# Kernel optimization log

Hardware: AMD Instinct MI355X
Metric: run time of the kernel (lower is better)

The kernel has to match this reference:

```python
import jax, jax.numpy as jnp
import numpy as np

B, S, DN, L = 2048, 8, 8, 50        # batch, n_sparse, n_dense, hist len
V, VF = 100000, 100000              # sparse vocab, feed vocab
ED, FD = 16, 512                    # sparse embed dim, feed embed dim
HID1, HID2 = 256, 128               # DNN hidden sizes
NE, NT, EO = 8, 4, 8                # experts, tasks, expert out dim
INPUT_DIM = ED * S + DN + FD + FD   # 1160


def setup_inputs() -> dict:
    key = jax.random.key(0)
    ks = jax.random.split(key, 20)
    sc = 0.02
    f32 = jnp.float32
    return {
        "sparse_ids": jax.random.randint(ks[0], (B, S), 0, V),
        "dense": jax.random.normal(ks[1], (B, DN), f32),
        "feedid": jax.random.randint(ks[2], (B,), 0, VF),
        "hist_feedid": jax.random.randint(ks[3], (B, L), 0, VF),
        "emb_tables": jax.random.normal(ks[4], (S, V, ED), f32) * sc,
        "feed_table": jax.random.normal(ks[5], (VF, FD), f32) * sc,
        "attn_w1": jax.random.normal(ks[6], (4 * FD, 128), f32) * sc,
        "attn_b1": jnp.zeros((128,), f32),
        "attn_w2": jax.random.normal(ks[7], (128, 1), f32) * sc,
        "attn_b2": jnp.zeros((1,), f32),
        "dnn_w1": jax.random.normal(ks[8], (INPUT_DIM, HID1), f32) * sc,
        "dnn_b1": jnp.zeros((HID1,), f32),
        "dnn_w2": jax.random.normal(ks[9], (HID1, HID2), f32) * sc,
        "dnn_b2": jnp.zeros((HID2,), f32),
        "expert_w": jax.random.normal(ks[10], (NE, HID2, EO), f32) * sc,
        "gate_w": jax.random.normal(ks[11], (NT, HID2, NE), f32) * sc,
        "out_w": jax.random.normal(ks[12], (NT, EO, 1), f32) * sc,
        "out_b": jnp.zeros((NT, 1), f32),
    }


def reference(sparse_ids, dense, feedid, hist_feedid,
              emb_tables, feed_table,
              attn_w1, attn_b1, attn_w2, attn_b2,
              dnn_w1, dnn_b1, dnn_w2, dnn_b2,
              expert_w, gate_w, out_w, out_b):
    # --- sparse embeddings: one table per feature -> [B, S, ED] -> flat ---
    embed = jax.vmap(lambda t, ids: t[ids], in_axes=(0, 1), out_axes=1)(
        emb_tables, sparse_ids)                       # [B, S, ED]
    sparse_flat = embed.reshape(embed.shape[0], -1)   # [B, S*ED]

    # --- feed / history embeddings ---
    feed = feed_table[feedid]                         # [B, FD]
    hist = feed_table[hist_feedid]                    # [B, L, FD]

    # --- DIN attention (query=feed, keys=hist) ---
    q = jnp.broadcast_to(feed[:, None, :], hist.shape)          # [B, L, FD]
    x = jnp.concatenate([q, hist, q - hist, q * hist], axis=-1)  # [B, L, 4FD]
    h = jax.nn.relu(x @ attn_w1 + attn_b1)                       # [B, L, 128]
    scores = (h @ attn_w2 + attn_b2)[..., 0]                     # [B, L]
    attn = jax.nn.softmax(scores, axis=1)
    user_interest = jnp.einsum('bl,bld->bd', attn, hist)         # [B, FD]

    # --- DNN (dropout off in eval) ---
    dnn_in = jnp.concatenate([sparse_flat, dense, feed, user_interest], axis=1)
    z = jax.nn.relu(dnn_in @ dnn_w1 + dnn_b1)
    dnn_out = jax.nn.relu(z @ dnn_w2 + dnn_b2)                   # [B, 128]

    # --- MMOE (eval: no expert dropout mask) ---
    expert_out = jnp.einsum('bi,eio->beo', dnn_out, expert_w)    # [B, NE, EO]
    gates = jax.nn.softmax(jnp.einsum('bi,tie->bte', dnn_out, gate_w), axis=-1)
    task_out = jnp.einsum('bte,beo->bto', gates, expert_out)     # [B, NT, EO]

    # --- per-task heads ---
    logits = jnp.einsum('bto,toh->bth', task_out, out_w) + out_b  # [B, NT, 1]
    return jax.nn.sigmoid(logits)
```

## Files before the change

### kernel.cpp

```cpp
#include <hip/hip_runtime.h>
#include <hip/hip_bf16.h>

typedef unsigned short u16;
typedef unsigned int u32;
typedef __attribute__((ext_vector_type(8))) short short8;
typedef __attribute__((ext_vector_type(8))) u16 ushort8;
typedef __attribute__((ext_vector_type(4))) float f32x4;

#define BB 2048
#define SS 8
#define DNUM 8
#define LL 50
#define EDIM 16
#define FDIM 512
#define HID1 256
#define HID2 128
#define VF 100000
#define KDNN 1216
#define ROWS (BB*LL)

__device__ inline u16 f2bf(float x) {
    return __builtin_bit_cast(u16, __float2bfloat16(x));
}
__device__ inline float bf2f(u16 b) {
    u32 u = ((u32)b) << 16;
    return __builtin_bit_cast(float, u);
}
__device__ inline void load16_lds(const void* g, void* l) {
    __builtin_amdgcn_global_load_lds(
        (const __attribute__((address_space(1))) u32*)g,
        (__attribute__((address_space(3))) u32*)l, 16, 0, 0);
}
__device__ inline float wave_sum(float v) {
    #pragma unroll
    for (int off = 32; off > 0; off >>= 1) v += __shfl_xor(v, off, 64);
    return v;
}
__device__ inline float wave_max(float v) {
    #pragma unroll
    for (int off = 32; off > 0; off >>= 1) v = fmaxf(v, __shfl_xor(v, off, 64));
    return v;
}
__device__ inline void cvt8(const float4& a, const float4& b, ushort8& o) {
    o[0]=f2bf(a.x); o[1]=f2bf(a.y); o[2]=f2bf(a.z); o[3]=f2bf(a.w);
    o[4]=f2bf(b.x); o[5]=f2bf(b.y); o[6]=f2bf(b.z); o[7]=f2bf(b.w);
}

__global__ __launch_bounds__(256) void zero_flags(u32* __restrict__ f) {
    int i = blockIdx.x * 256 + threadIdx.x;
    if (i < 25024) f[i] = 0;
}

__global__ __launch_bounds__(256) void mark_used(
    const int* __restrict__ hist, const int* __restrict__ feedid,
    unsigned char* __restrict__ flags)
{
    int i = blockIdx.x * 256 + threadIdx.x;
    if (i < ROWS) flags[hist[i]] = 1;
    if (i < BB) flags[feedid[i]] = 1;
}

#define CVT_BLKS 25000
#define PREP_BLKS 2112
__global__ __launch_bounds__(256) void prep_all(
    const float* __restrict__ ft, u16* __restrict__ hb,
    const unsigned char* __restrict__ flags,
    const float* __restrict__ w1, const float* __restrict__ dw1,
    const float* __restrict__ dw2,
    u16* __restrict__ WHP_T, u16* __restrict__ WQ_T,
    u16* __restrict__ W1D_T, u16* __restrict__ W2D_T,
    const int* __restrict__ sparse_ids, const float* __restrict__ dense,
    const int* __restrict__ feedid, const float* __restrict__ emb_tables,
    u16* __restrict__ dnn_in, u16* __restrict__ A_q)
{
    int blk = blockIdx.x, t = threadIdx.x;
    if (blk < CVT_BLKS) {
        int r = blk * 4 + (t >> 6);
        if (flags[r]) {
            const float* src = ft + (size_t)r * FDIM + (t & 63) * 8;
            float4 a = *(const float4*)src;
            float4 b = *(const float4*)(src + 4);
            ushort8 o; cvt8(a, b, o);
            *(ushort8*)(hb + (size_t)r * FDIM + (t & 63) * 8) = o;
        }
    } else if (blk < CVT_BLKS + PREP_BLKS) {
        int idx = (blk - CVT_BLKS) * 256 + t;
        if (idx < 131072) {
            int n = idx >> 10, k = idx & 1023;
            float v;
            if (k < 512) v = w1[(512 + k) * 128 + n] - w1[(1024 + k) * 128 + n];
            else         v = w1[(1024 + k) * 128 + n];
            WHP_T[n * 1024 + k] = f2bf(v);
        } else if (idx < 196608) {
            int i = idx - 131072;
            int n = i >> 9, k = i & 511;
            WQ_T[n * 512 + k] = f2bf(w1[k * 128 + n] + w1[(1024 + k) * 128 + n]);
        } else if (idx < 507904) {
            int i = idx - 196608;
            int n = i / KDNN, k = i - n * KDNN;
            W1D_T[i] = (k < 1160) ? f2bf(dw1[k * HID1 + n]) : (u16)0;
        } else if (idx < 540672) {
            int i = idx - 507904;
            int n = i >> 8, k = i & 255;
            W2D_T[i] = f2bf(dw2[k * HID2 + n]);
        }
    } else {
        int b = blk - (CVT_BLKS + PREP_BLKS);
        u16* drow = dnn_in + (size_t)b * KDNN;
        if (t < 128) {
            int s = t >> 4, e = t & 15;
            int id = sparse_ids[b * SS + s];
            float v = emb_tables[(size_t)s * 1600000 + (size_t)id * EDIM + e];
            drow[t] = f2bf(v);
        } else if (t < 136) {
            drow[t] = f2bf(dense[b * DNUM + (t - 128)]);
        } else if (t < 192) {
            drow[1160 + (t - 136)] = 0;
        }
        int fid = feedid[b];
        float2 f = *(const float2*)&ft[(size_t)fid * FDIM + t * 2];
        u16 u0 = f2bf(f.x), u1 = f2bf(f.y);
        drow[136 + t * 2] = u0;
        drow[136 + t * 2 + 1] = u1;
        A_q[(size_t)b * FDIM + t * 2] = u0;
        A_q[(size_t)b * FDIM + t * 2 + 1] = u1;
    }
}

template<int BM, bool RELU, bool OUT_BF16>
__global__ __launch_bounds__(256, 4) void gemm_bt(
    const u16* __restrict__ A, int lda,
    const u16* __restrict__ BT, int ldb,
    const float* __restrict__ bias,
    void* __restrict__ Cv, int M, int N, int K)
{
    constexpr int MI = BM / 32;
    __shared__ u16 As[BM * 64];
    __shared__ u16 Bs[128 * 64];
    int m0 = blockIdx.x * BM, n0 = blockIdx.y * 128;
    int tid = threadIdx.x, wave = tid >> 6, lane = tid & 63;
    int lrow = lane >> 3, lk = (lane & 7) * 8;
    f32x4 acc[MI][4];
    f32x4 zz = {0.f, 0.f, 0.f, 0.f};
    #pragma unroll
    for (int i = 0; i < MI; i++)
        #pragma unroll
        for (int j = 0; j < 4; j++) acc[i][j] = zz;
    int wm = (wave >> 1) * (BM / 2), wn = (wave & 1) * 64;

    for (int kt = 0; kt < K; kt += 64) {
        #pragma unroll
        for (int j = 0; j < MI; ++j) {
            int c = wave * MI + j;
            int row = c * 8 + lrow;
            load16_lds(A + (size_t)(m0 + row) * lda + kt + lk, &As[c * 512]);
        }
        #pragma unroll
        for (int j = 0; j < 4; ++j) {
            int c = wave * 4 + j;
            int row = c * 8 + lrow;
            load16_lds(BT + (size_t)(n0 + row) * ldb + kt + lk, &Bs[c * 512]);
        }
        __syncthreads();
        #pragma unroll
        for (int ks = 0; ks < 2; ++ks) {
            int kk = ks * 32 + (lane >> 4) * 8;
            short8 af[MI], bf[4];
            #pragma unroll
            for (int i = 0; i < MI; i++)
                af[i] = *(const short8*)&As[(wm + i * 16 + (lane & 15)) * 64 + kk];
            #pragma unroll
            for (int j = 0; j < 4; j++)
                bf[j] = *(const short8*)&Bs[(wn + j * 16 + (lane & 15)) * 64 + kk];
            #pragma unroll
            for (int i = 0; i < MI; i++)
                #pragma unroll
                for (int j = 0; j < 4; j++)
                    acc[i][j] = __builtin_amdgcn_mfma_f32_16x16x32_bf16(
                        af[i], bf[j], acc[i][j], 0, 0, 0);
        }
        __syncthreads();
    }
    #pragma unroll
    for (int i = 0; i < MI; i++) {
        #pragma unroll
        for (int j = 0; j < 4; j++) {
            #pragma unroll
            for (int r = 0; r < 4; r++) {
                int row = m0 + wm + i * 16 + (lane >> 4) * 4 + r;
                int col = n0 + wn + j * 16 + (lane & 15);
                float v = acc[i][j][r];
                if (bias) v += bias[col];
                if (RELU) v = fmaxf(v, 0.f);
                size_t off = (size_t)row * N + col;
                if (OUT_BF16) ((u16*)Cv)[off] = f2bf(v);
                else ((float*)Cv)[off] = v;
            }
        }
    }
}

#define MFMA_BF16 __builtin_amdgcn_mfma_f32_16x16x32_bf16

__global__ __launch_bounds__(256, 4) void din_gemm(
    const int* __restrict__ hist_ids, const int* __restrict__ feedid,
    const u16* __restrict__ HB, const u16* __restrict__ WHP_T,
    const float* __restrict__ qw, const float* __restrict__ b1,
    const float* __restrict__ w2v, float* __restrict__ scores)
{
    __shared__ u16 As[2][64 * 32];
    __shared__ u16 BsH[128 * 32];
    __shared__ u16 BsP[128 * 32];
    __shared__ u16 qls[3 * 512];
    __shared__ float qbs[3 * 128];
    __shared__ float w2s[128];
    __shared__ float sred[64 * 2];

    int t = threadIdx.x, w = t >> 6, lane = t & 63;
    int m0 = blockIdx.x * 64, b0 = m0 / LL;
    int fr = lane & 15, kg8 = (lane >> 4) * 8;
    int wm = (w >> 1) * 32, wn = (w & 1) * 64;

    for (int idx = t; idx < 384; idx += 256) {
        int bi = idx >> 7, col = idx & 127;
        int bb = b0 + bi; if (bb > BB - 1) bb = BB - 1;
        qbs[idx] = qw[bb * 128 + col] + b1[col];
    }
    if (t < 128) w2s[t] = w2v[t];

    const u16* a_src = HB + (size_t)hist_ids[m0 + w * 16 + (lane >> 2)] * FDIM
                          + (lane & 3) * 8;
    const u16* b_src0 = WHP_T + (size_t)(w * 32 + (lane >> 2)) * 1024 + (lane & 3) * 8;
    const u16* b_src1 = b_src0 + 16 * 1024;

    if (w < 3) {
        int bb = b0 + w; if (bb > BB - 1) bb = BB - 1;
        load16_lds(HB + (size_t)feedid[bb] * FDIM + lane * 8, &qls[w * 512]);
    }
    int qb0 = (m0 + wm + fr) / LL - b0;
    int qb1 = (m0 + wm + 16 + fr) / LL - b0;

    f32x4 acc[2][4];
    f32x4 zz = {0.f, 0.f, 0.f, 0.f};
    #pragma unroll
    for (int i = 0; i < 2; i++)
        #pragma unroll
        for (int j = 0; j < 4; j++) acc[i][j] = zz;

    load16_lds(a_src,         &As[0][w * 512]);
    load16_lds(b_src0,        &BsH[(w * 2) * 512]);
    load16_lds(b_src1,        &BsH[(w * 2 + 1) * 512]);
    load16_lds(b_src0 + 512,  &BsP[(w * 2) * 512]);
    load16_lds(b_src1 + 512,  &BsP[(w * 2 + 1) * 512]);
    load16_lds(a_src + 32,    &As[1][w * 512]);
    asm volatile("s_waitcnt vmcnt(1) lgkmcnt(0)" ::: "memory");
    __builtin_amdgcn_s_barrier();

    #pragma unroll
    for (int kt = 0; kt < 16; ++kt) {
        const int buf = kt & 1;
        const int ko = kt * 32;
        short8 ah0 = *(const short8*)&As[buf][(wm + fr) * 32 + kg8];
        short8 ah1 = *(const short8*)&As[buf][(wm + 16 + fr) * 32 + kg8];
        ushort8 qv0 = *(const ushort8*)&qls[qb0 * 512 + ko + kg8];
        ushort8 qv1 = *(const ushort8*)&qls[qb1 * 512 + ko + kg8];
        short8 bh[4], bp[4];
        #pragma unroll
        for (int j = 0; j < 4; ++j) {
            int n = wn + j * 16 + fr;
            bh[j] = *(const short8*)&BsH[n * 32 + kg8];
            bp[j] = *(const short8*)&BsP[n * 32 + kg8];
        }
        #pragma unroll
        for (int j = 0; j < 4; ++j) {
            acc[0][j] = MFMA_BF16(ah0, bh[j], acc[0][j], 0, 0, 0);
            acc[1][j] = MFMA_BF16(ah1, bh[j], acc[1][j], 0, 0, 0);
        }
        ushort8 hv0 = __builtin_bit_cast(ushort8, ah0);
        ushort8 hv1 = __builtin_bit_cast(ushort8, ah1);
        ushort8 pv0, pv1;
        #pragma unroll
        for (int e = 0; e < 8; ++e) {
            pv0[e] = f2bf(bf2f(hv0[e]) * bf2f(qv0[e]));
            pv1[e] = f2bf(bf2f(hv1[e]) * bf2f(qv1[e]));
        }
        short8 ap0 = __builtin_bit_cast(short8, pv0);
        short8 ap1 = __builtin_bit_cast(short8, pv1);
        #pragma unroll
        for (int j = 0; j < 4; ++j) {
            acc[0][j] = MFMA_BF16(ap0, bp[j], acc[0][j], 0, 0, 0);
            acc[1][j] = MFMA_BF16(ap1, bp[j], acc[1][j], 0, 0, 0);
        }
        asm volatile("s_waitcnt lgkmcnt(0)" ::: "memory");
        __builtin_amdgcn_s_barrier();
        if (kt < 15) {
            const int kn = (kt + 1) * 32;
            load16_lds(b_src0 + kn,       &BsH[(w * 2) * 512]);
            load16_lds(b_src1 + kn,       &BsH[(w * 2 + 1) * 512]);
            load16_lds(b_src0 + 512 + kn, &BsP[(w * 2) * 512]);
            load16_lds(b_src1 + 512 + kn, &BsP[(w * 2 + 1) * 512]);
            if (kt < 14) {
                load16_lds(a_src + (kt + 2) * 32, &As[buf][w * 512]);
                asm volatile("s_waitcnt vmcnt(1)" ::: "memory");
            } else {
                asm volatile("s_waitcnt vmcnt(0)" ::: "memory");
            }
            __builtin_amdgcn_s_barrier();
        }
    }

    #pragma unroll
    for (int i = 0; i < 2; ++i) {
        #pragma unroll
        for (int r = 0; r < 4; ++r) {
            int rl = wm + i * 16 + (lane >> 4) * 4 + r;
            int bi = (m0 + rl) / LL - b0;
            float s = 0.f;
            #pragma unroll
            for (int j = 0; j < 4; ++j) {
                int col = wn + j * 16 + fr;
                float v = acc[i][j][r] + qbs[bi * 128 + col];
                s += fmaxf(v, 0.f) * w2s[col];
            }
            s += __shfl_xor(s, 1, 64);
            s += __shfl_xor(s, 2, 64);
            s += __shfl_xor(s, 4, 64);
            s += __shfl_xor(s, 8, 64);
            if (fr == 0) sred[rl * 2 + (w & 1)] = s;
        }
    }
    __syncthreads();
    if (t < 64) scores[m0 + t] = sred[t * 2] + sred[t * 2 + 1];
}

__global__ __launch_bounds__(256) void softmax_ui(
    const float* __restrict__ scores, const int* __restrict__ hist_ids,
    const u16* __restrict__ HB, u16* __restrict__ dnn_in)
{
    int b = blockIdx.x, t = threadIdx.x;
    int wave = t >> 6, lane = t & 63;
    __shared__ float sc[56];
    __shared__ int hid[56];
    if (t >= 64 && t < 64 + LL) hid[t - 64] = hist_ids[b * LL + (t - 64)];
    if (wave == 0) {
        float x = (lane < LL) ? scores[b * LL + lane] : -1e30f;
        float mx = wave_max(x);
        float e = (lane < LL) ? __expf(x - mx) : 0.f;
        float s = wave_sum(e);
        if (lane < LL) sc[lane] = e / s;
    }
    __syncthreads();
    int d = t * 2;
    float a0 = 0.f, a1 = 0.f;
    #pragma unroll 5
    for (int l = 0; l < LL; ++l) {
        u32 v = *(const u32*)(HB + (size_t)hid[l] * FDIM + d);
        float al = sc[l];
        a0 += al * bf2f((u16)(v & 0xffff));
        a1 += al * bf2f((u16)(v >> 16));
    }
    dnn_in[(size_t)b * KDNN + 648 + d] = f2bf(a0);
    dnn_in[(size_t)b * KDNN + 648 + d + 1] = f2bf(a1);
}

__global__ __launch_bounds__(256) void mmoe_head(
    const float* __restrict__ dnn_out, const float* __restrict__ expert_w,
    const float* __restrict__ gate_w, const float* __restrict__ out_w,
    const float* __restrict__ out_b, float* __restrict__ out)
{
    int wave = threadIdx.x >> 6, lane = threadIdx.x & 63;
    int b = blockIdx.x * 4 + wave;
    __shared__ float ds[4][128];
    __shared__ float eo[4][64];
    __shared__ float gt[4][32];
    ds[wave][lane] = dnn_out[b * 128 + lane];
    ds[wave][lane + 64] = dnn_out[b * 128 + 64 + lane];
    __syncthreads();
    int e = lane >> 3, o = lane & 7;
    float acc = 0.f;
    for (int k = 0; k < 128; ++k)
        acc += ds[wave][k] * expert_w[(e * 128 + k) * 8 + o];
    eo[wave][lane] = acc;
    if (lane < 32) {
        int tt = lane >> 3, ee = lane & 7;
        float g = 0.f;
        for (int k = 0; k < 128; ++k)
            g += ds[wave][k] * gate_w[(tt * 128 + k) * 8 + ee];
        float m = g;
        #pragma unroll
        for (int off = 4; off; off >>= 1) m = fmaxf(m, __shfl_xor(m, off, 8));
        float ex = __expf(g - m);
        float s = ex;
        #pragma unroll
        for (int off = 4; off; off >>= 1) s += __shfl_xor(s, off, 8);
        gt[wave][lane] = ex / s;
    }
    __syncthreads();
    if (lane < 32) {
        int tt = lane >> 3, o2 = lane & 7;
        float to = 0.f;
        #pragma unroll
        for (int ee = 0; ee < 8; ++ee)
            to += gt[wave][tt * 8 + ee] * eo[wave][ee * 8 + o2];
        float pl = to * out_w[tt * 8 + o2];
        #pragma unroll
        for (int off = 4; off; off >>= 1) pl += __shfl_xor(pl, off, 8);
        if (o2 == 0) {
            float logit = pl + out_b[tt];
            out[b * 4 + tt] = 1.f / (1.f + __expf(-logit));
        }
    }
}

extern "C" void kernel_launch(void* const* d_in, const int* in_sizes, int n_in,
                              void* d_out, int out_size, void* d_ws, size_t ws_size,
                              hipStream_t stream)
{
    const int*   sparse_ids = (const int*)d_in[0];
    const float* dense      = (const float*)d_in[1];
    const int*   feedid     = (const int*)d_in[2];
    const int*   hist_ids   = (const int*)d_in[3];
    const float* emb_tables = (const float*)d_in[4];
    const float* feed_table = (const float*)d_in[5];
    const float* attn_w1    = (const float*)d_in[6];
    const float* attn_b1    = (const float*)d_in[7];
    const float* attn_w2    = (const float*)d_in[8];
    const float* attn_b2    = (const float*)d_in[9];
    const float* dnn_w1     = (const float*)d_in[10];
    const float* dnn_b1     = (const float*)d_in[11];
    const float* dnn_w2     = (const float*)d_in[12];
    const float* dnn_b2     = (const float*)d_in[13];
    const float* expert_w   = (const float*)d_in[14];
    const float* gate_w     = (const float*)d_in[15];
    const float* out_w      = (const float*)d_in[16];
    const float* out_b      = (const float*)d_in[17];
    float* out = (float*)d_out;

    char* ws = (char*)d_ws;
    size_t off = 0;
    auto alloc = [&](size_t bytes) {
        char* p = ws + off;
        off += (bytes + 255) & ~(size_t)255;
        return p;
    };
    u16* WHP_T = (u16*)alloc(131072 * 2);
    u16* WQ_T  = (u16*)alloc(65536 * 2);
    u16* W1D_T = (u16*)alloc((size_t)HID1 * KDNN * 2);
    u16* W2D_T = (u16*)alloc((size_t)HID2 * HID1 * 2);
    u16* AQ    = (u16*)alloc((size_t)BB * FDIM * 2);
    float* QW  = (float*)alloc((size_t)BB * 128 * 4);
    u16* DNNIN = (u16*)alloc((size_t)BB * KDNN * 2);
    u16* Z     = (u16*)alloc((size_t)BB * HID1 * 2);
    float* DOUT= (float*)alloc((size_t)BB * HID2 * 4);
    float* SCORES = (float*)alloc((size_t)ROWS * 4);
    unsigned char* FLAGS = (unsigned char*)alloc(100096);
    u16* HB16  = (u16*)alloc((size_t)VF * FDIM * 2);

    zero_flags<<<98, 256, 0, stream>>>((u32*)FLAGS);
    mark_used<<<400, 256, 0, stream>>>(hist_ids, feedid, FLAGS);
    prep_all<<<CVT_BLKS + PREP_BLKS + BB, 256, 0, stream>>>(
        feed_table, HB16, FLAGS, attn_w1, dnn_w1, dnn_w2,
        WHP_T, WQ_T, W1D_T, W2D_T,
        sparse_ids, dense, feedid, emb_tables, DNNIN, AQ);
    gemm_bt<32, false, false><<<dim3(BB / 32, 1), 256, 0, stream>>>(
        AQ, 512, WQ_T, 512, nullptr, QW, BB, 128, 512);
    din_gemm<<<ROWS / 64, 256, 0, stream>>>(
        hist_ids, feedid, HB16, WHP_T, QW, attn_b1, attn_w2, SCORES);
    softmax_ui<<<BB, 256, 0, stream>>>(SCORES, hist_ids, HB16, DNNIN);
    gemm_bt<32, true, true><<<dim3(BB / 32, HID1 / 128), 256, 0, stream>>>(
        DNNIN, KDNN, W1D_T, KDNN, dnn_b1, Z, BB, HID1, KDNN);
    gemm_bt<32, true, false><<<dim3(BB / 32, 1), 256, 0, stream>>>(
        Z, HID1, W2D_T, HID1, dnn_b2, DOUT, BB, HID2, HID1);
    mmoe_head<<<BB / 4, 256, 0, stream>>>(DOUT, expert_w, gate_w, out_w,
                                          out_b, out);
}
```

Baseline: 152.6 us.

## Gather fp32 feed rows directly in DIN GEMM instead of pre-converting table to bf16

Drops the flag-marking kernels and the pass that converted every used feed-table row to bf16 in a workspace copy. The DIN attention GEMM now streams fp32 history rows straight into LDS and converts them to bf16 in registers before the MFMA. The query rows and the softmax-weighted sum read the fp32 table too. This removes two launches and a large scan-and-write of the table, at the cost of twice the gather bytes per history row in the main GEMM and extra conversion work in its inner loop.

Result: no change. 150.2 us (-1.6%).

```diff
diff --git a/kernel.cpp b/kernel.cpp
--- a/kernel.cpp
+++ b/kernel.cpp
@@ -46,25 +46,9 @@
     o[4]=f2bf(b.x); o[5]=f2bf(b.y); o[6]=f2bf(b.z); o[7]=f2bf(b.w);
 }
 
-__global__ __launch_bounds__(256) void zero_flags(u32* __restrict__ f) {
-    int i = blockIdx.x * 256 + threadIdx.x;
-    if (i < 25024) f[i] = 0;
-}
-
-__global__ __launch_bounds__(256) void mark_used(
-    const int* __restrict__ hist, const int* __restrict__ feedid,
-    unsigned char* __restrict__ flags)
-{
-    int i = blockIdx.x * 256 + threadIdx.x;
-    if (i < ROWS) flags[hist[i]] = 1;
-    if (i < BB) flags[feedid[i]] = 1;
-}
-
-#define CVT_BLKS 25000
 #define PREP_BLKS 2112
-__global__ __launch_bounds__(256) void prep_all(
-    const float* __restrict__ ft, u16* __restrict__ hb,
-    const unsigned char* __restrict__ flags,
+__global__ __launch_bounds__(256) void prep_small(
+    const float* __restrict__ ft,
     const float* __restrict__ w1, const float* __restrict__ dw1,
     const float* __restrict__ dw2,
     u16* __restrict__ WHP_T, u16* __restrict__ WQ_T,
@@ -74,17 +58,8 @@
     u16* __restrict__ dnn_in, u16* __restrict__ A_q)
 {
     int blk = blockIdx.x, t = threadIdx.x;
-    if (blk < CVT_BLKS) {
-        int r = blk * 4 + (t >> 6);
-        if (flags[r]) {
-            const float* src = ft + (size_t)r * FDIM + (t & 63) * 8;
-            float4 a = *(const float4*)src;
-            float4 b = *(const float4*)(src + 4);
-            ushort8 o; cvt8(a, b, o);
-            *(ushort8*)(hb + (size_t)r * FDIM + (t & 63) * 8) = o;
-        }
-    } else if (blk < CVT_BLKS + PREP_BLKS) {
-        int idx = (blk - CVT_BLKS) * 256 + t;
+    if (blk < PREP_BLKS) {
+        int idx = blk * 256 + t;
         if (idx < 131072) {
             int n = idx >> 10, k = idx & 1023;
             float v;
@@ -105,7 +80,7 @@
             W2D_T[i] = f2bf(dw2[k * HID2 + n]);
         }
     } else {
-        int b = blk - (CVT_BLKS + PREP_BLKS);
+        int b = blk - PREP_BLKS;
         u16* drow = dnn_in + (size_t)b * KDNN;
         if (t < 128) {
             int s = t >> 4, e = t & 15;
@@ -204,11 +179,11 @@
 
 __global__ __launch_bounds__(256, 4) void din_gemm(
     const int* __restrict__ hist_ids, const int* __restrict__ feedid,
-    const u16* __restrict__ HB, const u16* __restrict__ WHP_T,
+    const float* __restrict__ ft, const u16* __restrict__ WHP_T,
     const float* __restrict__ qw, const float* __restrict__ b1,
     const float* __restrict__ w2v, float* __restrict__ scores)
 {
-    __shared__ u16 As[2][64 * 32];
+    __shared__ float Asf[2][64 * 32];
     __shared__ u16 BsH[128 * 32];
     __shared__ u16 BsP[128 * 32];
     __shared__ u16 qls[3 * 512];
@@ -227,16 +202,20 @@
         qbs[idx] = qw[bb * 128 + col] + b1[col];
     }
     if (t < 128) w2s[t] = w2v[t];
-
-    const u16* a_src = HB + (size_t)hist_ids[m0 + w * 16 + (lane >> 2)] * FDIM
-                          + (lane & 3) * 8;
+    for (int idx = t; idx < 768; idx += 256) {
+        int bi = idx >> 8, d2 = (idx & 255) * 2;
+        int bb = b0 + bi; if (bb > BB - 1) bb = BB - 1;
+        float2 qv = *(const float2*)&ft[(size_t)feedid[bb] * FDIM + d2];
+        qls[bi * 512 + d2] = f2bf(qv.x);
+        qls[bi * 512 + d2 + 1] = f2bf(qv.y);
+    }
+
+    const float* a_src0 = ft + (size_t)hist_ids[m0 + w * 16 + fr] * FDIM
+                             + (lane >> 4) * 4;
+    const float* a_src1 = a_src0 + 16;
     const u16* b_src0 = WHP_T + (size_t)(w * 32 + (lane >> 2)) * 1024 + (lane & 3) * 8;
     const u16* b_src1 = b_src0 + 16 * 1024;
 
-    if (w < 3) {
-        int bb = b0 + w; if (bb > BB - 1) bb = BB - 1;
-        load16_lds(HB + (size_t)feedid[bb] * FDIM + lane * 8, &qls[w * 512]);
-    }
     int qb0 = (m0 + wm + fr) / LL - b0;
     int qb1 = (m0 + wm + 16 + fr) / LL - b0;
 
@@ -247,21 +226,33 @@
         #pragma unroll
         for (int j = 0; j < 4; j++) acc[i][j] = zz;
 
-    load16_lds(a_src,         &As[0][w * 512]);
+    load16_lds(a_src0,        &Asf[0][w * 512]);
+    load16_lds(a_src1,        &Asf[0][w * 512 + 256]);
     load16_lds(b_src0,        &BsH[(w * 2) * 512]);
     load16_lds(b_src1,        &BsH[(w * 2 + 1) * 512]);
     load16_lds(b_src0 + 512,  &BsP[(w * 2) * 512]);
     load16_lds(b_src1 + 512,  &BsP[(w * 2 + 1) * 512]);
-    load16_lds(a_src + 32,    &As[1][w * 512]);
-    asm volatile("s_waitcnt vmcnt(1) lgkmcnt(0)" ::: "memory");
+    load16_lds(a_src0 + 32,   &Asf[1][w * 512]);
+    load16_lds(a_src1 + 32,   &Asf[1][w * 512 + 256]);
+    asm volatile("s_waitcnt vmcnt(2) lgkmcnt(0)" ::: "memory");
     __builtin_amdgcn_s_barrier();
+
+    int ws0 = wm >> 4;
+    int k4a = (lane >> 4) * 2;
+    int offA0 = ws0 * 512 + k4a * 64 + fr * 4;
+    int offA1 = (ws0 + 1) * 512 + k4a * 64 + fr * 4;
 
     #pragma unroll
     for (int kt = 0; kt < 16; ++kt) {
         const int buf = kt & 1;
         const int ko = kt * 32;
-        short8 ah0 = *(const short8*)&As[buf][(wm + fr) * 32 + kg8];
-        short8 ah1 = *(const short8*)&As[buf][(wm + 16 + fr) * 32 + kg8];
+        float4 h0a = *(const float4*)&Asf[buf][offA0];
+        float4 h0b = *(const float4*)&Asf[buf][offA0 + 64];
+        float4 h1a = *(const float4*)&Asf[buf][offA1];
+        float4 h1b = *(const float4*)&Asf[buf][offA1 + 64];
+        ushort8 hv0, hv1;
+        cvt8(h0a, h0b, hv0);
+        cvt8(h1a, h1b, hv1);
         ushort8 qv0 = *(const ushort8*)&qls[qb0 * 512 + ko + kg8];
         ushort8 qv1 = *(const ushort8*)&qls[qb1 * 512 + ko + kg8];
         short8 bh[4], bp[4];
@@ -271,13 +262,13 @@
             bh[j] = *(const short8*)&BsH[n * 32 + kg8];
             bp[j] = *(const short8*)&BsP[n * 32 + kg8];
         }
+        short8 ah0 = __builtin_bit_cast(short8, hv0);
+        short8 ah1 = __builtin_bit_cast(short8, hv1);
         #pragma unroll
         for (int j = 0; j < 4; ++j) {
             acc[0][j] = MFMA_BF16(ah0, bh[j], acc[0][j], 0, 0, 0);
             acc[1][j] = MFMA_BF16(ah1, bh[j], acc[1][j], 0, 0, 0);
         }
-        ushort8 hv0 = __builtin_bit_cast(ushort8, ah0);
-        ushort8 hv1 = __builtin_bit_cast(ushort8, ah1);
         ushort8 pv0, pv1;
         #pragma unroll
         for (int e = 0; e < 8; ++e) {
@@ -294,14 +285,16 @@
         asm volatile("s_waitcnt lgkmcnt(0)" ::: "memory");
         __builtin_amdgcn_s_barrier();
         if (kt < 15) {
-            const int kn = (kt + 1) * 32;
-            load16_lds(b_src0 + kn,       &BsH[(w * 2) * 512]);
-            load16_lds(b_src1 + kn,       &BsH[(w * 2 + 1) * 512]);
-            load16_lds(b_src0 + 512 + kn, &BsP[(w * 2) * 512]);
-            load16_lds(b_src1 + 512 + kn, &BsP[(w * 2 + 1) * 512]);
+            const int knB = (kt + 1) * 32;
+            load16_lds(b_src0 + knB,       &BsH[(w * 2) * 512]);
+            load16_lds(b_src1 + knB,       &BsH[(w * 2 + 1) * 512]);
+            load16_lds(b_src0 + 512 + knB, &BsP[(w * 2) * 512]);
+            load16_lds(b_src1 + 512 + knB, &BsP[(w * 2 + 1) * 512]);
             if (kt < 14) {
-                load16_lds(a_src + (kt + 2) * 32, &As[buf][w * 512]);
-                asm volatile("s_waitcnt vmcnt(1)" ::: "memory");
+                const int knA = (kt + 2) * 32;
+                load16_lds(a_src0 + knA, &Asf[buf][w * 512]);
+                load16_lds(a_src1 + knA, &Asf[buf][w * 512 + 256]);
+                asm volatile("s_waitcnt vmcnt(2)" ::: "memory");
             } else {
                 asm volatile("s_waitcnt vmcnt(0)" ::: "memory");
             }
@@ -335,7 +328,7 @@
 
 __global__ __launch_bounds__(256) void softmax_ui(
     const float* __restrict__ scores, const int* __restrict__ hist_ids,
-    const u16* __restrict__ HB, u16* __restrict__ dnn_in)
+    const float* __restrict__ feed_table, u16* __restrict__ dnn_in)
 {
     int b = blockIdx.x, t = threadIdx.x;
     int wave = t >> 6, lane = t & 63;
@@ -354,10 +347,10 @@
     float a0 = 0.f, a1 = 0.f;
     #pragma unroll 5
     for (int l = 0; l < LL; ++l) {
-        u32 v = *(const u32*)(HB + (size_t)hid[l] * FDIM + d);
+        float2 hv = *(const float2*)&feed_table[(size_t)hid[l] * FDIM + d];
         float al = sc[l];
-        a0 += al * bf2f((u16)(v & 0xffff));
-        a1 += al * bf2f((u16)(v >> 16));
+        a0 += al * hv.x;
+        a1 += al * hv.y;
     }
     dnn_in[(size_t)b * KDNN + 648 + d] = f2bf(a0);
     dnn_in[(size_t)b * KDNN + 648 + d + 1] = f2bf(a1);
@@ -435,6 +428,7 @@
     const float* out_w      = (const float*)d_in[16];
     const float* out_b      = (const float*)d_in[17];
     float* out = (float*)d_out;
+    (void)attn_b2;
 
     char* ws = (char*)d_ws;
     size_t off = 0;
@@ -453,20 +447,16 @@
     u16* Z     = (u16*)alloc((size_t)BB * HID1 * 2);
     float* DOUT= (float*)alloc((size_t)BB * HID2 * 4);
     float* SCORES = (float*)alloc((size_t)ROWS * 4);
-    unsigned char* FLAGS = (unsigned char*)alloc(100096);
-    u16* HB16  = (u16*)alloc((size_t)VF * FDIM * 2);
-
-    zero_flags<<<98, 256, 0, stream>>>((u32*)FLAGS);
-    mark_used<<<400, 256, 0, stream>>>(hist_ids, feedid, FLAGS);
-    prep_all<<<CVT_BLKS + PREP_BLKS + BB, 256, 0, stream>>>(
-        feed_table, HB16, FLAGS, attn_w1, dnn_w1, dnn_w2,
+
+    prep_small<<<PREP_BLKS + BB, 256, 0, stream>>>(
+        feed_table, attn_w1, dnn_w1, dnn_w2,
         WHP_T, WQ_T, W1D_T, W2D_T,
         sparse_ids, dense, feedid, emb_tables, DNNIN, AQ);
     gemm_bt<32, false, false><<<dim3(BB / 32, 1), 256, 0, stream>>>(
         AQ, 512, WQ_T, 512, nullptr, QW, BB, 128, 512);
     din_gemm<<<ROWS / 64, 256, 0, stream>>>(
-        hist_ids, feedid, HB16, WHP_T, QW, attn_b1, attn_w2, SCORES);
-    softmax_ui<<<BB, 256, 0, stream>>>(SCORES, hist_ids, HB16, DNNIN);
+        hist_ids, feedid, feed_table, WHP_T, QW, attn_b1, attn_w2, SCORES);
+    softmax_ui<<<BB, 256, 0, stream>>>(SCORES, hist_ids, feed_table, DNNIN);
     gemm_bt<32, true, true><<<dim3(BB / 32, HID1 / 128), 256, 0, stream>>>(
         DNNIN, KDNN, W1D_T, KDNN, dnn_b1, Z, BB, HID1, KDNN);
     gemm_bt<32, true, false><<<dim3(BB / 32, 1), 256, 0, stream>>>(
```
